# Kernel tuning notes

Hardware: AMD Instinct MI355X
Metric: run time of the kernel (lower is better)

## Reference

```python
import jax, jax.numpy as jnp
import numpy as np

B, FIN, N, E = 4, 354, 4096, 65536
HID, HEADS, PH = 352, 4, 88  # per_head = gat_hidden // num_heads
EPS = 1e-5
NEG_SLOPE = 0.2  # GATConv leaky_relu slope


def setup_inputs() -> dict:
    key = jax.random.key(0)
    ks = jax.random.split(key, 32)
    s = 0.05
    inp = {
        "x": jax.random.normal(ks[0], (B, FIN, N), dtype=jnp.float32),
        "edge_index": jax.random.randint(ks[1], (2, E), 0, N, dtype=jnp.int32),
        # GATConv 1: in=354 -> heads*per_head=352
        "W1": jax.random.normal(ks[2], (FIN, HID), dtype=jnp.float32) * s,
        "att_src1": jax.random.normal(ks[3], (HEADS, PH), dtype=jnp.float32) * s,
        "att_dst1": jax.random.normal(ks[4], (HEADS, PH), dtype=jnp.float32) * s,
        "b1": jnp.zeros((HID,), jnp.float32),
        "gn1_w": jnp.ones((HID,), jnp.float32),
        "gn1_b": jnp.zeros((HID,), jnp.float32),
        "gn1_ms": jnp.ones((HID,), jnp.float32),
        # GATConv 2
        "W2": jax.random.normal(ks[5], (HID, HID), dtype=jnp.float32) * s,
        "att_src2": jax.random.normal(ks[6], (HEADS, PH), dtype=jnp.float32) * s,
        "att_dst2": jax.random.normal(ks[7], (HEADS, PH), dtype=jnp.float32) * s,
        "b2": jnp.zeros((HID,), jnp.float32),
        "gn2_w": jnp.ones((HID,), jnp.float32),
        "gn2_b": jnp.zeros((HID,), jnp.float32),
        "gn2_ms": jnp.ones((HID,), jnp.float32),
        # GATConv 3
        "W3": jax.random.normal(ks[8], (HID, HID), dtype=jnp.float32) * s,
        "att_src3": jax.random.normal(ks[9], (HEADS, PH), dtype=jnp.float32) * s,
        "att_dst3": jax.random.normal(ks[10], (HEADS, PH), dtype=jnp.float32) * s,
        "b3": jnp.zeros((HID,), jnp.float32),
        "gn3_w": jnp.ones((HID,), jnp.float32),
        "gn3_b": jnp.zeros((HID,), jnp.float32),
        "gn3_ms": jnp.ones((HID,), jnp.float32),
        # classifier Linear(352 -> 1)
        "clf_w": jax.random.normal(ks[11], (1, HID), dtype=jnp.float32) * s,
        "clf_b": jnp.zeros((1,), jnp.float32),
    }
    return inp


def reference(x, edge_index, W1, att_src1, att_dst1, b1, gn1_w, gn1_b, gn1_ms,
              W2, att_src2, att_dst2, b2, gn2_w, gn2_b, gn2_ms,
              W3, att_src3, att_dst3, b3, gn3_w, gn3_b, gn3_ms,
              clf_w, clf_b):
    n = x.shape[2]
    h_in = jnp.transpose(x, (0, 2, 1))  # [B, N, FIN]
    # PyG GATConv default add_self_loops=True
    loop = jnp.arange(n, dtype=edge_index.dtype)
    src = jnp.concatenate([edge_index[0], loop])
    dst = jnp.concatenate([edge_index[1], loop])

    def gat(h, W, a_s, a_d, b):  # h: [N, Fin]
        H, C = a_s.shape
        xh = (h @ W).reshape(n, H, C)                      # [N, H, C]
        a_src = jnp.sum(xh * a_s, axis=-1)                 # [N, H]
        a_dst = jnp.sum(xh * a_d, axis=-1)                 # [N, H]
        logits = jax.nn.leaky_relu(a_src[src] + a_dst[dst], NEG_SLOPE)  # [Etot, H]
        m = jax.ops.segment_max(logits, dst, num_segments=n)
        ex = jnp.exp(logits - m[dst])
        den = jax.ops.segment_sum(ex, dst, num_segments=n)
        alpha = ex / den[dst]                              # segment softmax over in-edges
        out = jax.ops.segment_sum(xh[src] * alpha[:, :, None], dst, num_segments=n)
        return out.reshape(n, H * C) + b

    def gnorm(h, w, b, ms):  # GraphNorm over a single graph
        mu = jnp.mean(h, axis=0)
        o = h - ms * mu
        var = jnp.mean(o * o, axis=0)
        return o / jnp.sqrt(var + EPS) * w + b

    def per_graph(h):
        h1 = jax.nn.relu(gnorm(gat(h, W1, att_src1, att_dst1, b1), gn1_w, gn1_b, gn1_ms))
        h2 = jax.nn.relu(gnorm(gat(h1, W2, att_src2, att_dst2, b2), gn2_w, gn2_b, gn2_ms) + h1)
        h3 = jax.nn.relu(gnorm(gat(h2, W3, att_src3, att_dst3, b3), gn3_w, gn3_b, gn3_ms) + h2)
        return jnp.mean(h3, axis=0)  # global_mean_pool

    pooled = jax.vmap(per_graph)(h_in)  # [B, HID]
    return pooled @ clf_w.T + clf_b     # [B, 1]
```

## Files before the change

### kernel.cpp

```cpp
#include <hip/hip_runtime.h>
#include <math.h>

#define N_NODES 4096
#define B_GR 4
#define FIN_K 354
#define K1P 384
#define HID 352
#define NHEAD 4
#define PH 88
#define E_EDGES 65536
#define ETOT (E_EDGES + N_NODES)
#define EPSV 1e-5f
#define SLOPE 0.2f
#define SPLITS 64

typedef unsigned short u16;
typedef unsigned int u32;
typedef __attribute__((ext_vector_type(8))) short bf16x8;
typedef __attribute__((ext_vector_type(4))) float f32x4;

__device__ __forceinline__ void split_bf16(float v, u16& hi, u16& lo) {
    u32 u = __float_as_uint(v);
    hi = (u16)(u >> 16);
    float rem = v - __uint_as_float(((u32)hi) << 16);
    lo = (u16)(__float_as_uint(rem) >> 16);
}

__device__ __forceinline__ u16 bf16_rne(float v) {
    u32 u = __float_as_uint(v);
    u32 r = u + 0x7FFFu + ((u >> 16) & 1u);
    return (u16)(r >> 16);
}

__global__ void k_zero_int(int* p, int n) {
    int i = blockIdx.x * blockDim.x + threadIdx.x;
    if (i < n) p[i] = 0;
}

__global__ void k_hist(const int* __restrict__ ei, int* __restrict__ cnt) {
    int e = blockIdx.x * blockDim.x + threadIdx.x;
    if (e >= ETOT) return;
    int dst = (e < E_EDGES) ? ei[E_EDGES + e] : (e - E_EDGES);
    atomicAdd(&cnt[dst], 1);
}

__global__ void k_scan(const int* __restrict__ cnt, int* __restrict__ rp) {
    __shared__ int tot[256];
    int t = threadIdx.x;
    int base = t * 16;
    int loc[16];
    int s = 0;
    #pragma unroll
    for (int i = 0; i < 16; i++) { loc[i] = s; s += cnt[base + i]; }
    tot[t] = s;
    __syncthreads();
    for (int off = 1; off < 256; off <<= 1) {
        int v = (t >= off) ? tot[t - off] : 0;
        __syncthreads();
        tot[t] += v;
        __syncthreads();
    }
    int excl = (t == 0) ? 0 : tot[t - 1];
    #pragma unroll
    for (int i = 0; i < 16; i++) rp[base + i] = excl + loc[i];
    if (t == 255) rp[N_NODES] = tot[255];
}

__global__ void k_scatter(const int* __restrict__ ei, const int* __restrict__ rp,
                          int* __restrict__ cur, int* __restrict__ col) {
    int e = blockIdx.x * blockDim.x + threadIdx.x;
    if (e >= ETOT) return;
    int src, dst;
    if (e < E_EDGES) { src = ei[e]; dst = ei[E_EDGES + e]; }
    else { src = e - E_EDGES; dst = src; }
    int pos = rp[dst] + atomicAdd(&cur[dst], 1);
    col[pos] = src;
}

__global__ __launch_bounds__(256) void k_prep_x(const float* __restrict__ x,
                                                u16* __restrict__ xth, u16* __restrict__ xtl) {
    __shared__ float tile[64][65];
    int b = blockIdx.z;
    int n0 = blockIdx.x * 64;
    int k0 = blockIdx.y * 64;
    int tid = threadIdx.x;
    int r = tid >> 2;
    int cq = (tid & 3) * 16;
    int kglob = k0 + r;
    if (kglob < FIN_K) {
        const float* src = x + ((size_t)b * FIN_K + kglob) * N_NODES + n0 + cq;
        float4 v0 = *reinterpret_cast<const float4*>(src + 0);
        float4 v1 = *reinterpret_cast<const float4*>(src + 4);
        float4 v2 = *reinterpret_cast<const float4*>(src + 8);
        float4 v3 = *reinterpret_cast<const float4*>(src + 12);
        *reinterpret_cast<float4*>(&tile[r][cq + 0]) = v0;
        *reinterpret_cast<float4*>(&tile[r][cq + 4]) = v1;
        *reinterpret_cast<float4*>(&tile[r][cq + 8]) = v2;
        *reinterpret_cast<float4*>(&tile[r][cq + 12]) = v3;
    } else {
        float4 z = make_float4(0.f, 0.f, 0.f, 0.f);
        *reinterpret_cast<float4*>(&tile[r][cq + 0]) = z;
        *reinterpret_cast<float4*>(&tile[r][cq + 4]) = z;
        *reinterpret_cast<float4*>(&tile[r][cq + 8]) = z;
        *reinterpret_cast<float4*>(&tile[r][cq + 12]) = z;
    }
    __syncthreads();
    int nr = tid >> 2;
    int kq = (tid & 3) * 16;
    u16 hb[16], lb[16];
    #pragma unroll
    for (int i = 0; i < 16; i++) split_bf16(tile[kq + i][nr], hb[i], lb[i]);
    size_t o = ((size_t)b * N_NODES + n0 + nr) * K1P + k0 + kq;
    *reinterpret_cast<uint4*>(xth + o)     = *reinterpret_cast<uint4*>(hb);
    *reinterpret_cast<uint4*>(xth + o + 8) = *reinterpret_cast<uint4*>(hb + 8);
    *reinterpret_cast<uint4*>(xtl + o)     = *reinterpret_cast<uint4*>(lb);
    *reinterpret_cast<uint4*>(xtl + o + 8) = *reinterpret_cast<uint4*>(lb + 8);
}

__global__ void k_prep_w(const float* __restrict__ W, u16* __restrict__ wth, u16* __restrict__ wtl,
                         int K, int KP) {
    int n = blockIdx.x;
    for (int k = threadIdx.x; k < KP; k += 64) {
        float v = 0.f;
        if (n < HID && k < K) v = W[(size_t)k * HID + n];
        u16 hi, lo;
        split_bf16(v, hi, lo);
        wth[(size_t)n * KP + k] = hi;
        wtl[(size_t)n * KP + k] = lo;
    }
}

__global__ __launch_bounds__(256) void k_gemm_mfma(
    const u16* __restrict__ Ah, const u16* __restrict__ Al,
    const u16* __restrict__ Bh, const u16* __restrict__ Bl,
    float* __restrict__ C, int K)
{
    __shared__ __align__(16) char smem[24576];
    const int AHo = 0, ALo = 4096, BHo = 8192, BLo = 16384;
    int b = blockIdx.z;
    int m0 = blockIdx.y * 64;
    int n0 = blockIdx.x * 128;
    int tid = threadIdx.x;
    int lane = tid & 63, wid = tid >> 6;
    int wr = (wid >> 1) * 32, wc = (wid & 1) * 64;
    int lrow = lane & 15, kgv = lane >> 4;

    const u16* Abh = Ah + (size_t)b * N_NODES * K;
    const u16* Abl = Al + (size_t)b * N_NODES * K;

    int srow = tid >> 2, skg = tid & 3;
    int sxor = (srow >> 1) & 3;
    int st_lds = srow * 64 + ((skg ^ sxor) << 4);
    int st_lds1 = (srow + 64) * 64 + ((skg ^ sxor) << 4);
    size_t a_g  = (size_t)(m0 + srow) * K + skg * 8;
    size_t b_g0 = (size_t)(n0 + srow) * K + skg * 8;
    size_t b_g1 = (size_t)(n0 + srow + 64) * K + skg * 8;

    int a_ad[2], b_ad[4];
    #pragma unroll
    for (int mf = 0; mf < 2; mf++) {
        int r = wr + mf * 16 + lrow;
        a_ad[mf] = r * 64 + ((kgv ^ ((r >> 1) & 3)) << 4);
    }
    #pragma unroll
    for (int nf = 0; nf < 4; nf++) {
        int c = wc + nf * 16 + lrow;
        b_ad[nf] = c * 64 + ((kgv ^ ((c >> 1) & 3)) << 4);
    }

    f32x4 acc[2][4];
    #pragma unroll
    for (int i = 0; i < 2; i++)
        #pragma unroll
        for (int j = 0; j < 4; j++) acc[i][j] = (f32x4){0.f, 0.f, 0.f, 0.f};

    uint4 cah = *(const uint4*)(Abh + a_g);
    uint4 cal = *(const uint4*)(Abl + a_g);
    uint4 cbh0 = *(const uint4*)(Bh + b_g0);
    uint4 cbl0 = *(const uint4*)(Bl + b_g0);
    uint4 cbh1 = *(const uint4*)(Bh + b_g1);
    uint4 cbl1 = *(const uint4*)(Bl + b_g1);

    for (int k0 = 0; k0 < K; k0 += 32) {
        __syncthreads();
        *(uint4*)(smem + AHo + st_lds) = cah;
        *(uint4*)(smem + ALo + st_lds) = cal;
        *(uint4*)(smem + BHo + st_lds) = cbh0;
        *(uint4*)(smem + BLo + st_lds) = cbl0;
        *(uint4*)(smem + BHo + st_lds1) = cbh1;
        *(uint4*)(smem + BLo + st_lds1) = cbl1;
        int k1 = k0 + 32;
        uint4 nah, nal, nbh0, nbl0, nbh1, nbl1;
        bool more = k1 < K;
        if (more) {
            nah = *(const uint4*)(Abh + a_g + k1);
            nal = *(const uint4*)(Abl + a_g + k1);
            nbh0 = *(const uint4*)(Bh + b_g0 + k1);
            nbl0 = *(const uint4*)(Bl + b_g0 + k1);
            nbh1 = *(const uint4*)(Bh + b_g1 + k1);
            nbl1 = *(const uint4*)(Bl + b_g1 + k1);
        }
        __syncthreads();

        bf16x8 fah0 = *(const bf16x8*)(smem + AHo + a_ad[0]);
        bf16x8 fah1 = *(const bf16x8*)(smem + AHo + a_ad[1]);
        bf16x8 fal0 = *(const bf16x8*)(smem + ALo + a_ad[0]);
        bf16x8 fal1 = *(const bf16x8*)(smem + ALo + a_ad[1]);
        #pragma unroll
        for (int nf = 0; nf < 4; nf++) {
            bf16x8 fbh = *(const bf16x8*)(smem + BHo + b_ad[nf]);
            bf16x8 fbl = *(const bf16x8*)(smem + BLo + b_ad[nf]);
            acc[0][nf] = __builtin_amdgcn_mfma_f32_16x16x32_bf16(fah0, fbh, acc[0][nf], 0, 0, 0);
            acc[1][nf] = __builtin_amdgcn_mfma_f32_16x16x32_bf16(fah1, fbh, acc[1][nf], 0, 0, 0);
            acc[0][nf] = __builtin_amdgcn_mfma_f32_16x16x32_bf16(fal0, fbh, acc[0][nf], 0, 0, 0);
            acc[1][nf] = __builtin_amdgcn_mfma_f32_16x16x32_bf16(fal1, fbh, acc[1][nf], 0, 0, 0);
            acc[0][nf] = __builtin_amdgcn_mfma_f32_16x16x32_bf16(fah0, fbl, acc[0][nf], 0, 0, 0);
            acc[1][nf] = __builtin_amdgcn_mfma_f32_16x16x32_bf16(fah1, fbl, acc[1][nf], 0, 0, 0);
        }
        if (more) { cah = nah; cal = nal; cbh0 = nbh0; cbl0 = nbl0; cbh1 = nbh1; cbl1 = nbl1; }
    }

    #pragma unroll
    for (int nf = 0; nf < 4; nf++) {
        int colg = n0 + wc + nf * 16 + lrow;
        if (colg < HID) {
            #pragma unroll
            for (int mf = 0; mf < 2; mf++) {
                #pragma unroll
                for (int r = 0; r < 4; r++) {
                    int rowg = m0 + wr + mf * 16 + kgv * 4 + r;
                    C[((size_t)b * N_NODES + rowg) * HID + colg] = acc[mf][nf][r];
                }
            }
        }
    }
}

__global__ void k_att(const float* __restrict__ xh,
                      const float* __restrict__ as_, const float* __restrict__ ad_,
                      float* __restrict__ osrc, float* __restrict__ odst,
                      u16* __restrict__ xb16) {
    int idx = blockIdx.x * blockDim.x + threadIdx.x;
    if (idx >= B_GR * N_NODES * NHEAD) return;
    int h = idx & 3;
    int bn = idx >> 2;
    const float* base = xh + (size_t)bn * HID + h * PH;
    const float* a1 = as_ + h * PH;
    const float* a2 = ad_ + h * PH;
    float s1 = 0.f, s2 = 0.f;
    u16 packed[PH];
    #pragma unroll
    for (int c = 0; c < PH; c += 4) {
        float4 v = *reinterpret_cast<const float4*>(&base[c]);
        float4 w1 = *reinterpret_cast<const float4*>(&a1[c]);
        float4 w2 = *reinterpret_cast<const float4*>(&a2[c]);
        s1 += v.x * w1.x + v.y * w1.y + v.z * w1.z + v.w * w1.w;
        s2 += v.x * w2.x + v.y * w2.y + v.z * w2.z + v.w * w2.w;
        packed[c + 0] = bf16_rne(v.x);
        packed[c + 1] = bf16_rne(v.y);
        packed[c + 2] = bf16_rne(v.z);
        packed[c + 3] = bf16_rne(v.w);
    }
    osrc[idx] = s1;
    odst[idx] = s2;
    u16* dstp = xb16 + (size_t)idx * PH;
    #pragma unroll
    for (int i = 0; i < PH; i += 8)
        *reinterpret_cast<uint4*>(dstp + i) = *reinterpret_cast<uint4*>(packed + i);
}

__global__ __launch_bounds__(256) void k_agg(
    const u16* __restrict__ xb16, const float* __restrict__ asrc,
    const float* __restrict__ adst, const int* __restrict__ rp,
    const int* __restrict__ col, const float* __restrict__ bias,
    float* __restrict__ g)
{
    int id = blockIdx.x;
    int xcd = id & 7;
    int gr = xcd >> 1;
    int dst = ((id >> 3) << 1) | (xcd & 1);
    int t = threadIdx.x;
    int h = t & 3, slot = t >> 2;
    int wave = t >> 6, lane = t & 63;
    int beg = rp[dst], end = rp[dst + 1];
    int deg = end - beg;
    const float* asG = asrc + (size_t)gr * N_NODES * NHEAD;
    float my_adst = adst[(size_t)gr * N_NODES * NHEAD + dst * 4 + h];

    __shared__ float s_e[64][4];
    __shared__ int s_src[64];
    __shared__ float s_m4[4][4];
    __shared__ float s_inv[4];

    int hh = t / 44;
    float2 acc = {0.f, 0.f};
    float den = 0.f;
    const u32* xb = reinterpret_cast<const u32*>(xb16) + (size_t)gr * N_NODES * 176;

    for (int c0 = 0; c0 < deg; c0 += 64) {
        int nthis = min(64, deg - c0);
        if (slot < nthis) {
            int s = col[beg + c0 + slot];
            if (h == 0) s_src[slot] = s;
            float x = asG[s * 4 + h] + my_adst;
            float lg = (x > 0.f) ? x : SLOPE * x;
            float e = expf(lg);
            s_e[slot][h] = e;
            den += e;
        }
        __syncthreads();
        if (t < 176) {
            #pragma unroll 4
            for (int i = 0; i < nthis; i++) {
                u32 v = xb[(size_t)s_src[i] * 176 + t];
                float a = s_e[i][hh];
                acc.x = fmaf(a, __uint_as_float(v << 16), acc.x);
                acc.y = fmaf(a, __uint_as_float(v & 0xFFFF0000u), acc.y);
            }
        }
        __syncthreads();
    }

    den += __shfl_xor(den, 4);
    den += __shfl_xor(den, 8);
    den += __shfl_xor(den, 16);
    den += __shfl_xor(den, 32);
    if (lane < 4) s_m4[wave][h] = den;
    __syncthreads();
    if (t < 4)
        s_inv[t] = 1.0f / (s_m4[0][t] + s_m4[1][t] + s_m4[2][t] + s_m4[3][t]);
    __syncthreads();

    if (t < 176) {
        float inv = s_inv[hh];
        int cc = t * 2;
        float2 o = {acc.x * inv + bias[cc], acc.y * inv + bias[cc + 1]};
        *reinterpret_cast<float2*>(&g[((size_t)gr * N_NODES + dst) * HID + cc]) = o;
    }
}

__global__ __launch_bounds__(384) void k_reduce(const float* __restrict__ g,
                                                float* __restrict__ ps, float* __restrict__ pss) {
    int b = blockIdx.y, chunk = blockIdx.x;
    int c = threadIdx.x;
    if (c >= HID) return;
    const int ROWS = N_NODES / SPLITS;
    int n0 = chunk * ROWS;
    const float* base = g + ((size_t)b * N_NODES + n0) * HID + c;
    float s = 0.f, ss = 0.f;
    for (int r = 0; r < ROWS; r++) {
        float v = base[(size_t)r * HID];
        s += v;
        ss = fmaf(v, v, ss);
    }
    ps[((size_t)b * SPLITS + chunk) * HID + c] = s;
    pss[((size_t)b * SPLITS + chunk) * HID + c] = ss;
}

__global__ void k_norm_final(const float* __restrict__ ps, const float* __restrict__ pss,
                             const float* __restrict__ ms, const float* __restrict__ w,
                             float* __restrict__ mu_ms, float* __restrict__ scale) {
    int b = blockIdx.x;
    int c = threadIdx.x;
    if (c >= HID) return;
    float s = 0.f, ss = 0.f;
    for (int q = 0; q < SPLITS; q++) {
        s += ps[((size_t)b * SPLITS + q) * HID + c];
        ss += pss[((size_t)b * SPLITS + q) * HID + c];
    }
    float mu = s / (float)N_NODES;
    float Eh2 = ss / (float)N_NODES;
    float msv = ms[c];
    float var = Eh2 - 2.f * msv * mu * mu + msv * msv * mu * mu;
    float rstd = 1.0f / sqrtf(var + EPSV);
    mu_ms[b * HID + c] = msv * mu;
    scale[b * HID + c] = rstd * w[c];
}

template<bool RES, bool WBF>
__global__ void k_apply(const float* __restrict__ g, const float* __restrict__ hprev,
                        const float* __restrict__ mu_ms, const float* __restrict__ scale,
                        const float* __restrict__ gnb, float* __restrict__ hout,
                        u16* __restrict__ hh, u16* __restrict__ hl) {
    size_t idx = (size_t)blockIdx.x * blockDim.x + threadIdx.x;
    size_t total = (size_t)B_GR * N_NODES * HID;
    if (idx >= total) return;
    int c = (int)(idx % HID);
    int b = (int)(idx / ((size_t)N_NODES * HID));
    float v = g[idx];
    float o = (v - mu_ms[b * HID + c]) * scale[b * HID + c] + gnb[c];
    if (RES) o += hprev[idx];
    o = fmaxf(o, 0.f);
    hout[idx] = o;
    if (WBF) {
        u16 hi, lo;
        split_bf16(o, hi, lo);
        hh[idx] = hi;
        hl[idx] = lo;
    }
}

__global__ __launch_bounds__(384) void k_final(const float* __restrict__ ps,
                                               const float* __restrict__ clfw,
                                               const float* __restrict__ clfb,
                                               float* __restrict__ out) {
    int b = blockIdx.x;
    int t = threadIdx.x;
    __shared__ float buf[384];
    float v = 0.f;
    if (t < HID) {
        float s = 0.f;
        for (int q = 0; q < SPLITS; q++) s += ps[((size_t)b * SPLITS + q) * HID + t];
        v = (s / (float)N_NODES) * clfw[t];
    }
    buf[t] = v;
    __syncthreads();
    if (t < 64) {
        float acc = 0.f;
        for (int j = t; j < 384; j += 64) acc += buf[j];
        for (int off = 32; off; off >>= 1) acc += __shfl_down(acc, off);
        if (t == 0) out[b] = acc + clfb[0];
    }
}

extern "C" void kernel_launch(void* const* d_in, const int* in_sizes, int n_in,
                              void* d_out, int out_size, void* d_ws, size_t ws_size,
                              hipStream_t stream) {
    const float* x = (const float*)d_in[0];
    const int* ei = (const int*)d_in[1];
    const float* W[3]   = {(const float*)d_in[2],  (const float*)d_in[9],  (const float*)d_in[16]};
    const float* as_[3] = {(const float*)d_in[3],  (const float*)d_in[10], (const float*)d_in[17]};
    const float* ad_[3] = {(const float*)d_in[4],  (const float*)d_in[11], (const float*)d_in[18]};
    const float* bi[3]  = {(const float*)d_in[5],  (const float*)d_in[12], (const float*)d_in[19]};
    const float* gw[3]  = {(const float*)d_in[6],  (const float*)d_in[13], (const float*)d_in[20]};
    const float* gb[3]  = {(const float*)d_in[7],  (const float*)d_in[14], (const float*)d_in[21]};
    const float* gms[3] = {(const float*)d_in[8],  (const float*)d_in[15], (const float*)d_in[22]};
    const float* clfw = (const float*)d_in[23];
    const float* clfb = (const float*)d_in[24];
    float* out = (float*)d_out;

    char* ws = (char*)d_ws;
    size_t off = 0;
    auto alloc = [&](size_t bytes) -> void* {
        void* p = ws + off;
        off += (bytes + 255) & ~(size_t)255;
        return p;
    };
    size_t bigf = sizeof(float) * (size_t)B_GR * N_NODES * HID;
    float* xh    = (float*)alloc(bigf);
    float* gbuf  = xh;
    float* hA    = (float*)alloc(bigf);
    float* hB    = (float*)alloc(bigf);
    size_t bfbytes = sizeof(u16) * (size_t)B_GR * N_NODES * K1P;
    u16* bf_hi = (u16*)alloc(bfbytes);
    u16* bf_lo = (u16*)alloc(bfbytes);
    u16* xb16  = (u16*)alloc(sizeof(u16) * (size_t)B_GR * N_NODES * NHEAD * PH);
    u16* wt_h[3]; u16* wt_l[3];
    wt_h[0] = (u16*)alloc(sizeof(u16) * 384 * K1P);
    wt_l[0] = (u16*)alloc(sizeof(u16) * 384 * K1P);
    for (int l = 1; l < 3; l++) {
        wt_h[l] = (u16*)alloc(sizeof(u16) * 384 * HID);
        wt_l[l] = (u16*)alloc(sizeof(u16) * 384 * HID);
    }
    float* a_s   = (float*)alloc(sizeof(float) * B_GR * N_NODES * NHEAD);
    float* a_d   = (float*)alloc(sizeof(float) * B_GR * N_NODES * NHEAD);
    float* ps    = (float*)alloc(sizeof(float) * B_GR * SPLITS * HID);
    float* pss   = (float*)alloc(sizeof(float) * B_GR * SPLITS * HID);
    float* mu_ms = (float*)alloc(sizeof(float) * B_GR * HID);
    float* scale = (float*)alloc(sizeof(float) * B_GR * HID);
    int* rp  = (int*)alloc(sizeof(int) * (N_NODES + 1));
    int* cnt = (int*)alloc(sizeof(int) * N_NODES);
    int* col = (int*)alloc(sizeof(int) * ETOT);

    k_prep_w<<<384, 64, 0, stream>>>(W[0], wt_h[0], wt_l[0], FIN_K, K1P);
    k_prep_w<<<384, 64, 0, stream>>>(W[1], wt_h[1], wt_l[1], HID, HID);
    k_prep_w<<<384, 64, 0, stream>>>(W[2], wt_h[2], wt_l[2], HID, HID);
    k_prep_x<<<dim3(64, 6, B_GR), 256, 0, stream>>>(x, bf_hi, bf_lo);

    k_zero_int<<<(N_NODES + 255) / 256, 256, 0, stream>>>(cnt, N_NODES);
    k_hist<<<(ETOT + 255) / 256, 256, 0, stream>>>(ei, cnt);
    k_scan<<<1, 256, 0, stream>>>(cnt, rp);
    k_zero_int<<<(N_NODES + 255) / 256, 256, 0, stream>>>(cnt, N_NODES);
    k_scatter<<<(ETOT + 255) / 256, 256, 0, stream>>>(ei, rp, cnt, col);

    const float* hin = nullptr;
    float* hcur = hA;
    dim3 ggrid(3, N_NODES / 64, B_GR);
    dim3 rgrid(SPLITS, B_GR);
    size_t total = (size_t)B_GR * N_NODES * HID;
    int ablocks = (int)((total + 255) / 256);

    for (int l = 0; l < 3; l++) {
        int K = (l == 0) ? K1P : HID;
        k_gemm_mfma<<<ggrid, 256, 0, stream>>>(bf_hi, bf_lo, wt_h[l], wt_l[l], xh, K);
        k_att<<<(B_GR * N_NODES * NHEAD + 255) / 256, 256, 0, stream>>>(xh, as_[l], ad_[l], a_s, a_d, xb16);
        k_agg<<<B_GR * N_NODES, 256, 0, stream>>>(xb16, a_s, a_d, rp, col, bi[l], gbuf);
        k_reduce<<<rgrid, 384, 0, stream>>>(gbuf, ps, pss);
        k_norm_final<<<B_GR, 384, 0, stream>>>(ps, pss, gms[l], gw[l], mu_ms, scale);
        if (l == 0)      k_apply<false, true ><<<ablocks, 256, 0, stream>>>(gbuf, nullptr, mu_ms, scale, gb[l], hcur, bf_hi, bf_lo);
        else if (l == 1) k_apply<true,  true ><<<ablocks, 256, 0, stream>>>(gbuf, hin, mu_ms, scale, gb[l], hcur, bf_hi, bf_lo);
        else             k_apply<true,  false><<<ablocks, 256, 0, stream>>>(gbuf, hin, mu_ms, scale, gb[l], hcur, bf_hi, bf_lo);
        hin = hcur;
        hcur = (hcur == hA) ? hB : hA;
    }
    k_reduce<<<rgrid, 384, 0, stream>>>(hin, ps, pss);
    k_final<<<B_GR, 384, 0, stream>>>(ps, clfw, clfb, out);
}
```

Baseline: 329.9 us.

## Assign one wavefront per destination node in GAT aggregation, removing block syncs

The aggregation kernel now gives each 64-lane wave its own destination node, four nodes per 256-thread block, instead of one node per block. Edge weights and source offsets are passed with wave shuffles rather than shared memory, so all __syncthreads barriers go away. Each lane now covers two or three feature pairs, which keeps every lane busy instead of leaving 80 of 256 threads idle during accumulation. The cost is more shuffles per edge and a 16-edge chunk size, and the two-level block-to-node mapping must still cover every node exactly once.

Result: faster. 319.3 us (-3.2%).

```diff
diff --git a/kernel.cpp b/kernel.cpp
--- a/kernel.cpp
+++ b/kernel.cpp
@@ -278,64 +278,69 @@
     int id = blockIdx.x;
     int xcd = id & 7;
     int gr = xcd >> 1;
-    int dst = ((id >> 3) << 1) | (xcd & 1);
-    int t = threadIdx.x;
-    int h = t & 3, slot = t >> 2;
-    int wave = t >> 6, lane = t & 63;
-    int beg = rp[dst], end = rp[dst + 1];
-    int deg = end - beg;
+    int w = threadIdx.x >> 6;
+    int l = threadIdx.x & 63;
+    int dst = ((((id >> 3) << 1) | (xcd & 1)) << 2) + w;
+    int h = l & 3, slot = l >> 2;
+    int beg = rp[dst];
+    int deg = rp[dst + 1] - beg;
     const float* asG = asrc + (size_t)gr * N_NODES * NHEAD;
-    float my_adst = adst[(size_t)gr * N_NODES * NHEAD + dst * 4 + h];
-
-    __shared__ float s_e[64][4];
-    __shared__ int s_src[64];
-    __shared__ float s_m4[4][4];
-    __shared__ float s_inv[4];
-
-    int hh = t / 44;
-    float2 acc = {0.f, 0.f};
+    float my_adst = adst[((size_t)gr * N_NODES + dst) * 4 + h];
+    const u32* xb = reinterpret_cast<const u32*>(xb16) + (size_t)gr * N_NODES * 176;
+
+    int c1 = l + 64, c2 = l + 128;
+    int hh0 = l / 44, hh1 = c1 / 44, hh2 = c2 / 44;
+    bool has2 = (l < 48);
+    float2 a0 = {0.f, 0.f}, a1 = {0.f, 0.f}, a2 = {0.f, 0.f};
     float den = 0.f;
-    const u32* xb = reinterpret_cast<const u32*>(xb16) + (size_t)gr * N_NODES * 176;
-
-    for (int c0 = 0; c0 < deg; c0 += 64) {
-        int nthis = min(64, deg - c0);
-        if (slot < nthis) {
-            int s = col[beg + c0 + slot];
-            if (h == 0) s_src[slot] = s;
-            float x = asG[s * 4 + h] + my_adst;
-            float lg = (x > 0.f) ? x : SLOPE * x;
-            float e = expf(lg);
-            s_e[slot][h] = e;
-            den += e;
-        }
-        __syncthreads();
-        if (t < 176) {
-            #pragma unroll 4
-            for (int i = 0; i < nthis; i++) {
-                u32 v = xb[(size_t)s_src[i] * 176 + t];
-                float a = s_e[i][hh];
-                acc.x = fmaf(a, __uint_as_float(v << 16), acc.x);
-                acc.y = fmaf(a, __uint_as_float(v & 0xFFFF0000u), acc.y);
+
+    for (int c0 = 0; c0 < deg; c0 += 16) {
+        int nthis = min(16, deg - c0);
+        int sIdx = col[beg + c0 + ((slot < nthis) ? slot : 0)];
+        float xv = asG[sIdx * 4 + h] + my_adst;
+        float lg = (xv > 0.f) ? xv : SLOPE * xv;
+        float e = (slot < nthis) ? expf(lg) : 0.f;
+        den += e;
+        int off = sIdx * 176;
+        #pragma unroll 2
+        for (int i = 0; i < nthis; i++) {
+            int offi = __shfl(off, i << 2);
+            float e0 = __shfl(e, (i << 2) | hh0);
+            float e1 = __shfl(e, (i << 2) | hh1);
+            u32 v0 = xb[offi + l];
+            u32 v1 = xb[offi + c1];
+            a0.x = fmaf(e0, __uint_as_float(v0 << 16), a0.x);
+            a0.y = fmaf(e0, __uint_as_float(v0 & 0xFFFF0000u), a0.y);
+            a1.x = fmaf(e1, __uint_as_float(v1 << 16), a1.x);
+            a1.y = fmaf(e1, __uint_as_float(v1 & 0xFFFF0000u), a1.y);
+            if (has2) {
+                float e2 = __shfl(e, (i << 2) | hh2);
+                u32 v2 = xb[offi + c2];
+                a2.x = fmaf(e2, __uint_as_float(v2 << 16), a2.x);
+                a2.y = fmaf(e2, __uint_as_float(v2 & 0xFFFF0000u), a2.y);
             }
         }
-        __syncthreads();
     }
 
     den += __shfl_xor(den, 4);
     den += __shfl_xor(den, 8);
     den += __shfl_xor(den, 16);
     den += __shfl_xor(den, 32);
-    if (lane < 4) s_m4[wave][h] = den;
-    __syncthreads();
-    if (t < 4)
-        s_inv[t] = 1.0f / (s_m4[0][t] + s_m4[1][t] + s_m4[2][t] + s_m4[3][t]);
-    __syncthreads();
-
-    if (t < 176) {
-        float inv = s_inv[hh];
-        int cc = t * 2;
-        float2 o = {acc.x * inv + bias[cc], acc.y * inv + bias[cc + 1]};
-        *reinterpret_cast<float2*>(&g[((size_t)gr * N_NODES + dst) * HID + cc]) = o;
+    float inv = 1.0f / den;
+    float i0 = __shfl(inv, hh0);
+    float i1 = __shfl(inv, hh1);
+    float* grow = g + ((size_t)gr * N_NODES + dst) * HID;
+    float2 b0 = *reinterpret_cast<const float2*>(bias + 2 * l);
+    float2 b1 = *reinterpret_cast<const float2*>(bias + 2 * c1);
+    float2 o0 = {a0.x * i0 + b0.x, a0.y * i0 + b0.y};
+    float2 o1 = {a1.x * i1 + b1.x, a1.y * i1 + b1.y};
+    *reinterpret_cast<float2*>(grow + 2 * l) = o0;
+    *reinterpret_cast<float2*>(grow + 2 * c1) = o1;
+    if (has2) {
+        float i2 = __shfl(inv, hh2);
+        float2 b2 = *reinterpret_cast<const float2*>(bias + 2 * c2);
+        float2 o2 = {a2.x * i2 + b2.x, a2.y * i2 + b2.y};
+        *reinterpret_cast<float2*>(grow + 2 * c2) = o2;
     }
 }
 
@@ -494,7 +499,7 @@
         int K = (l == 0) ? K1P : HID;
         k_gemm_mfma<<<ggrid, 256, 0, stream>>>(bf_hi, bf_lo, wt_h[l], wt_l[l], xh, K);
         k_att<<<(B_GR * N_NODES * NHEAD + 255) / 256, 256, 0, stream>>>(xh, as_[l], ad_[l], a_s, a_d, xb16);
-        k_agg<<<B_GR * N_NODES, 256, 0, stream>>>(xb16, a_s, a_d, rp, col, bi[l], gbuf);
+        k_agg<<<B_GR * N_NODES / 4, 256, 0, stream>>>(xb16, a_s, a_d, rp, col, bi[l], gbuf);
         k_reduce<<<rgrid, 384, 0, stream>>>(gbuf, ps, pss);
         k_norm_final<<<B_GR, 384, 0, stream>>>(ps, pss, gms[l], gw[l], mu_ms, scale);
         if (l == 0)      k_apply<false, true ><<<ablocks, 256, 0, stream>>>(gbuf, nullptr, mu_ms, scale, gb[l], hcur, bf_hi, bf_lo);
```
